# Performance work log

Hardware: AMD Instinct MI355X
Metric: run time of the kernel (lower is better)

The kernel has to match this reference:

```python
import jax, jax.numpy as jnp
import numpy as np

EPS = 1e-6          # VN leaky-relu denominator eps (vn_layers.py)
NEG_SLOPE = 0.2     # VNLinearLeakyReLU default negative_slope
K = 3               # pointops.interpolation default k
DIST_EPS = 1e-8     # interpolation inverse-distance eps


def vn_linear_leakyrelu(x, w_feat, w_dir):
    # x: [B, Cin, 3, N]; w_*: [Cout, Cin]  (bias-free Linears over channel dim)
    p = jnp.einsum('oc,bcvn->bovn', w_feat, x)
    d = jnp.einsum('oc,bcvn->bovn', w_dir, x)
    dot = jnp.sum(p * d, axis=2, keepdims=True)          # [B,Cout,1,N]
    d2 = jnp.sum(d * d, axis=2, keepdims=True)
    mask = (dot >= 0).astype(x.dtype)
    proj = p - (dot / (d2 + EPS)) * d                    # reflect negative part onto plane perp to d
    return NEG_SLOPE * p + (1.0 - NEG_SLOPE) * (mask * p + (1.0 - mask) * proj)


def interpolation(p2, p1, feat, b, n2, n1):
    # p2: [b*n2,3] coarse coords, p1: [b*n1,3] fine coords, feat: [C,3,b*n2]
    # k-NN inverse-squared-distance interpolation, segment-local per cloud.
    C = feat.shape[0]
    p2b = p2.reshape(b, n2, 3)
    p1b = p1.reshape(b, n1, 3)
    featb = feat.reshape(C * 3, b, n2).transpose(1, 2, 0)  # [b, n2, C*3]

    def per_batch(q, s, f):
        d2 = jnp.sum((q[:, None, :] - s[None, :, :]) ** 2, axis=-1)  # [n1,n2]
        neg_d2, idx = jax.lax.top_k(-d2, K)                          # k smallest sq-dists
        w = 1.0 / (-neg_d2 + DIST_EPS)
        w = w / jnp.sum(w, axis=1, keepdims=True)                    # [n1,K]
        return jnp.einsum('nk,nkc->nc', w, f[idx])                   # [n1, C*3]

    out = jax.vmap(per_batch)(p1b, p2b, featb)                       # [b, n1, C*3]
    return out.reshape(b, n1, C, 3).transpose(2, 3, 0, 1).reshape(C, 3, b * n1)


def setup_inputs() -> dict:
    key = jax.random.key(0)
    ks = jax.random.split(key, 8)
    b, n1, n2 = 4, 16384, 4096
    in_planes, out_planes = 128, 64
    p1 = jax.random.uniform(ks[0], (b * n1, 3), dtype=jnp.float32)
    p2 = jax.random.uniform(ks[1], (b * n2, 3), dtype=jnp.float32)
    x1 = jax.random.normal(ks[2], (1, out_planes, 3, b * n1), dtype=jnp.float32)
    x2 = jax.random.normal(ks[3], (1, in_planes, 3, b * n2), dtype=jnp.float32)
    o1 = (jnp.arange(1, b + 1, dtype=jnp.int32)) * n1   # cumulative offsets
    o2 = (jnp.arange(1, b + 1, dtype=jnp.int32)) * n2
    s1 = 1.0 / np.sqrt(out_planes)
    s2 = 1.0 / np.sqrt(in_planes)
    w1_feat = jax.random.uniform(ks[4], (out_planes, out_planes), jnp.float32, -s1, s1)
    w1_dir = jax.random.uniform(ks[5], (out_planes, out_planes), jnp.float32, -s1, s1)
    w2_feat = jax.random.uniform(ks[6], (out_planes, in_planes), jnp.float32, -s2, s2)
    w2_dir = jax.random.uniform(ks[7], (out_planes, in_planes), jnp.float32, -s2, s2)
    return {"p1": p1, "x1": x1, "o1": o1, "p2": p2, "x2": x2, "o2": o2,
            "w1_feat": w1_feat, "w1_dir": w1_dir, "w2_feat": w2_feat, "w2_dir": w2_dir}


def reference(p1, x1, o1, p2, x2, o2, w1_feat, w1_dir, w2_feat, w2_dir):
    b = o1.shape[0]
    n1 = x1.shape[-1] // b
    n2 = x2.shape[-1] // b
    y1 = vn_linear_leakyrelu(x1, w1_feat, w1_dir)            # [1,Cout,3,N1]
    y2 = vn_linear_leakyrelu(x2, w2_feat, w2_dir)[0]         # squeeze(0) -> [Cout,3,N2]
    up = interpolation(p2, p1, y2, b, n2, n1)                # [Cout,3,N1]
    return y1 + up
```

## Files before the change

kernel.cpp:

```cpp
#include <hip/hip_runtime.h>

#define N1T 65536
#define N2T 16384
#define COUT 64
#define CH 192
#define GRD 8
#define HCELL 0.125f

typedef unsigned short bhalf;
typedef __attribute__((ext_vector_type(8))) short short8;
typedef __attribute__((ext_vector_type(4))) float f32x4;

__device__ __forceinline__ bhalf f2bf(float f) {
    unsigned u = __float_as_uint(f);
    return (bhalf)((u + 0x7FFFu + ((u >> 16) & 1u)) >> 16);
}
__device__ __forceinline__ float bf2f(bhalf h) {
    return __uint_as_float(((unsigned)h) << 16);
}

__global__ __launch_bounds__(256) void wconv_kernel(
    const float* __restrict__ w1f, const float* __restrict__ w1d,
    const float* __restrict__ w2f, const float* __restrict__ w2d,
    bhalf* __restrict__ o1fh, bhalf* __restrict__ o1fl,
    bhalf* __restrict__ o1dh, bhalf* __restrict__ o1dl,
    bhalf* __restrict__ o2fh, bhalf* __restrict__ o2fl,
    bhalf* __restrict__ o2dh, bhalf* __restrict__ o2dl) {
    const int i = blockIdx.x * 256 + threadIdx.x;
    if (i < 4096) {
        const float a = w1f[i]; const bhalf ah = f2bf(a);
        o1fh[i] = ah; o1fl[i] = f2bf(a - bf2f(ah));
        const float b = w1d[i]; const bhalf bh = f2bf(b);
        o1dh[i] = bh; o1dl[i] = f2bf(b - bf2f(bh));
    }
    const float a = w2f[i]; const bhalf ah = f2bf(a);
    o2fh[i] = ah; o2fl[i] = f2bf(a - bf2f(ah));
    const float b = w2d[i]; const bhalf bh = f2bf(b);
    o2dh[i] = bh; o2dl[i] = f2bf(b - bf2f(bh));
}

template<int CIN, int N, bool CM>
__global__ __launch_bounds__(512) void vn_mfma_kernel(
    const float* __restrict__ x,
    const bhalf* __restrict__ wfh, const bhalf* __restrict__ wfl,
    const bhalf* __restrict__ wdh, const bhalf* __restrict__ wdl,
    const int*   __restrict__ idxs,
    const float* __restrict__ wts,
    const float* __restrict__ y2t,
    float* __restrict__ out)
{
    constexpr int ROWS = CIN * 3;
    constexpr int LDSC = CIN * 3 + 8;
    __shared__ __align__(16) bhalf xs_h[32][LDSC];
    __shared__ __align__(16) bhalf xs_l[32][LDSC];

    const int tid  = threadIdx.x;
    const int lane = tid & 63;
    const int wave = tid >> 6;
    const int n0   = blockIdx.x * 32;
    const int r16  = lane & 15;
    const int hh   = lane >> 4;
    const int ot   = wave & 3;
    const int sW   = wave >> 2;
    const int pt   = sW * 16 + r16;
    const int n    = n0 + pt;

    int gk[3]; float gw[3];
    if constexpr (CM) {
#pragma unroll
        for (int r = 0; r < 3; ++r) {
            gk[r] = idxs[r * N1T + n];
            gw[r] = wts[r * N1T + n];
        }
    }

    constexpr int NF4 = ROWS * 8;
    for (int i4 = tid; i4 < NF4; i4 += 512) {
        const int row = i4 >> 3, p4 = i4 & 7;
        const float4 v = *(const float4*)&x[(size_t)row * N + n0 + p4 * 4];
        const int c = row / 3, vv = row - c * 3;
        const int colS = (vv * CIN + c) ^ ((p4 & 3) << 3);
        const float vals[4] = {v.x, v.y, v.z, v.w};
#pragma unroll
        for (int j = 0; j < 4; ++j) {
            const bhalf h = f2bf(vals[j]);
            xs_h[p4*4+j][colS] = h;
            xs_l[p4*4+j][colS] = f2bf(vals[j] - bf2f(h));
        }
    }
    __syncthreads();

    const f32x4 zero = {0.f, 0.f, 0.f, 0.f};
    f32x4 accP[3], accD[3];
#pragma unroll
    for (int v = 0; v < 3; ++v) { accP[v] = zero; accD[v] = zero; }

    const int wofs = (ot * 16 + r16) * CIN + hh * 8;
    const bhalf* __restrict__ pfh = wfh + wofs;
    const bhalf* __restrict__ pfl = wfl + wofs;
    const bhalf* __restrict__ pdh = wdh + wofs;
    const bhalf* __restrict__ pdl = wdl + wofs;

    const int hs = ((hh ^ (r16 >> 2)) & 3) * 8 + (hh & ~3) * 8;
#pragma unroll
    for (int k = 0; k < CIN / 32; ++k) {
        const short8 afh = *(const short8*)(pfh + k * 32);
        const short8 afl = *(const short8*)(pfl + k * 32);
        const short8 adh = *(const short8*)(pdh + k * 32);
        const short8 adl = *(const short8*)(pdl + k * 32);
#pragma unroll
        for (int v = 0; v < 3; ++v) {
            const short8 bh = *(const short8*)&xs_h[pt][v * CIN + k * 32 + hs];
            const short8 bl = *(const short8*)&xs_l[pt][v * CIN + k * 32 + hs];
            accP[v] = __builtin_amdgcn_mfma_f32_16x16x32_bf16(afh, bh, accP[v], 0, 0, 0);
            accP[v] = __builtin_amdgcn_mfma_f32_16x16x32_bf16(afl, bh, accP[v], 0, 0, 0);
            accP[v] = __builtin_amdgcn_mfma_f32_16x16x32_bf16(afh, bl, accP[v], 0, 0, 0);
            accD[v] = __builtin_amdgcn_mfma_f32_16x16x32_bf16(adh, bh, accD[v], 0, 0, 0);
            accD[v] = __builtin_amdgcn_mfma_f32_16x16x32_bf16(adl, bh, accD[v], 0, 0, 0);
            accD[v] = __builtin_amdgcn_mfma_f32_16x16x32_bf16(adh, bl, accD[v], 0, 0, 0);
        }
    }

    float rr[12];
#pragma unroll
    for (int reg = 0; reg < 4; ++reg) {
        const float p0 = accP[0][reg], p1 = accP[1][reg], p2 = accP[2][reg];
        const float q0 = accD[0][reg], q1 = accD[1][reg], q2 = accD[2][reg];
        const float dot = p0*q0 + p1*q1 + p2*q2;
        const float dd  = q0*q0 + q1*q1 + q2*q2;
        const float coef = (dot < 0.f) ? (0.8f * dot / (dd + 1e-6f)) : 0.f;
        rr[reg*3+0] = p0 - coef * q0;
        rr[reg*3+1] = p1 - coef * q1;
        rr[reg*3+2] = p2 - coef * q2;
    }

    if constexpr (!CM) {
        float* op = out + (size_t)n * CH + ot * 48 + hh * 12;
        *(float4*)&op[0] = make_float4(rr[0], rr[1], rr[2],  rr[3]);
        *(float4*)&op[4] = make_float4(rr[4], rr[5], rr[6],  rr[7]);
        *(float4*)&op[8] = make_float4(rr[8], rr[9], rr[10], rr[11]);
    } else {
        const int chb = ot * 48 + hh * 12;
        const float* __restrict__ r0 = y2t + (size_t)gk[0] * CH + chb;
        const float* __restrict__ r1 = y2t + (size_t)gk[1] * CH + chb;
        const float* __restrict__ r2 = y2t + (size_t)gk[2] * CH + chb;
        const float w0 = gw[0], w1 = gw[1], w2 = gw[2];
        float4 a0[3], a1[3], a2[3];
#pragma unroll
        for (int q = 0; q < 3; ++q) {
            a0[q] = *(const float4*)&r0[q * 4];
            a1[q] = *(const float4*)&r1[q * 4];
            a2[q] = *(const float4*)&r2[q * 4];
        }
#pragma unroll
        for (int q = 0; q < 3; ++q) {
            const float u0 = w0*a0[q].x + w1*a1[q].x + w2*a2[q].x;
            const float u1 = w0*a0[q].y + w1*a1[q].y + w2*a2[q].y;
            const float u2 = w0*a0[q].z + w1*a1[q].z + w2*a2[q].z;
            const float u3 = w0*a0[q].w + w1*a1[q].w + w2*a2[q].w;
            out[(size_t)(chb + q*4 + 0) * N + n] = rr[q*4+0] + u0;
            out[(size_t)(chb + q*4 + 1) * N + n] = rr[q*4+1] + u1;
            out[(size_t)(chb + q*4 + 2) * N + n] = rr[q*4+2] + u2;
            out[(size_t)(chb + q*4 + 3) * N + n] = rr[q*4+3] + u3;
        }
    }
}

#define KNN_INSERT(d2, j)                                        \
    {                                                            \
        const bool c0 = (d2) < b0;                               \
        const bool c1 = (d2) < b1;                               \
        const bool c2 = (d2) < b2v;                              \
        const float nb2 = c2 ? (c1 ? b1 : (d2)) : b2v;           \
        const int   ni2 = c2 ? (c1 ? i1 : (j))  : i2;            \
        const float nb1 = c1 ? (c0 ? b0 : (d2)) : b1;            \
        const int   ni1 = c1 ? (c0 ? i0 : (j))  : i1;            \
        b0 = c0 ? (d2) : b0;  i0 = c0 ? (j) : i0;                \
        b1 = nb1; i1 = ni1; b2v = nb2; i2 = ni2;                 \
    }

__global__ __launch_bounds__(256) void zero_kernel(int* __restrict__ p, int n) {
    const int i = blockIdx.x * 256 + threadIdx.x;
    if (i < n) p[i] = 0;
}

__device__ __forceinline__ int cell_of(float x, float y, float z) {
    int cx = (int)(x * (float)GRD); cx = cx < 0 ? 0 : (cx > GRD-1 ? GRD-1 : cx);
    int cy = (int)(y * (float)GRD); cy = cy < 0 ? 0 : (cy > GRD-1 ? GRD-1 : cy);
    int cz = (int)(z * (float)GRD); cz = cz < 0 ? 0 : (cz > GRD-1 ? GRD-1 : cz);
    return (cz << 6) | (cy << 3) | cx;
}

__global__ __launch_bounds__(256) void bin_count_kernel(
    const float* __restrict__ p2, int* __restrict__ counts) {
    const int i = blockIdx.x * 256 + threadIdx.x;
    const float x = p2[i*3+0], y = p2[i*3+1], z = p2[i*3+2];
    const int cell = ((i >> 12) << 9) | cell_of(x, y, z);
    atomicAdd(&counts[cell], 1);
}

__global__ __launch_bounds__(256) void scan_kernel(
    const int* __restrict__ counts, int* __restrict__ off) {
    __shared__ int buf[2][256];
    const int t = threadIdx.x;
    int v[8]; int s = 0;
#pragma unroll
    for (int j = 0; j < 8; ++j) { const int tmp = counts[t*8+j]; v[j] = s; s += tmp; }
    buf[0][t] = s; __syncthreads();
    int src = 0;
    for (int d = 1; d < 256; d <<= 1) {
        int val = buf[src][t];
        if (t >= d) val += buf[src][t - d];
        buf[src ^ 1][t] = val; src ^= 1; __syncthreads();
    }
    const int incl = buf[src][t];
    const int base = incl - s;
#pragma unroll
    for (int j = 0; j < 8; ++j) off[t*8+j] = base + v[j];
    if (t == 255) off[2048] = incl;
}

__global__ __launch_bounds__(256) void bin_scatter_kernel(
    const float* __restrict__ p2, const int* __restrict__ off,
    int* __restrict__ cnt2, float4* __restrict__ binned) {
    const int i = blockIdx.x * 256 + threadIdx.x;
    const float x = p2[i*3+0], y = p2[i*3+1], z = p2[i*3+2];
    const int cell = ((i >> 12) << 9) | cell_of(x, y, z);
    const int pos = off[cell] + atomicAdd(&cnt2[cell], 1);
    binned[pos] = make_float4(x, y, z, __int_as_float(i));
}

__global__ __launch_bounds__(256) void knn_grid_kernel(
    const float* __restrict__ p1,
    const float4* __restrict__ binned,
    const int* __restrict__ off,
    int*   __restrict__ idx_out,
    float* __restrict__ w_out)
{
    const int t   = blockIdx.x * 256 + threadIdx.x;
    const int fp  = t >> 2;
    const int sub = t & 3;
    const int bi  = fp >> 14;
    const int cbase = bi << 9;

    const float qx = p1[fp*3+0], qy = p1[fp*3+1], qz = p1[fp*3+2];
    int cx = (int)(qx * (float)GRD); cx = cx < 0 ? 0 : (cx > 7 ? 7 : cx);
    int cy = (int)(qy * (float)GRD); cy = cy < 0 ? 0 : (cy > 7 ? 7 : cy);
    int cz = (int)(qz * (float)GRD); cz = cz < 0 ? 0 : (cz > 7 ? 7 : cz);

    float b0 = 1e30f, b1 = 1e30f, b2v = 1e30f;
    int   i0 = 0,     i1 = 0,     i2 = 0;

    for (int dz = -1; dz <= 1; ++dz)
    for (int dy = -1; dy <= 1; ++dy)
    for (int dx = -1; dx <= 1; ++dx) {
        const int nx = cx + dx, ny = cy + dy, nz = cz + dz;
        if ((unsigned)nx > 7u || (unsigned)ny > 7u || (unsigned)nz > 7u) continue;
        const int c = cbase + (nz << 6) + (ny << 3) + nx;
        const int s = off[c], e = off[c + 1];
        for (int k = s + sub; k < e; k += 4) {
            const float4 c4 = binned[k];
            const float ddx = qx - c4.x, ddy = qy - c4.y, ddz = qz - c4.z;
            const float d2 = fmaf(ddx, ddx, fmaf(ddy, ddy, ddz * ddz));
            const int j = __float_as_int(c4.w);
            KNN_INSERT(d2, j)
        }
    }

#pragma unroll
    for (int m = 1; m <= 2; m <<= 1) {
        const float c0v = __shfl_xor(b0, m, 4);
        const float c1v = __shfl_xor(b1, m, 4);
        const float c2v = __shfl_xor(b2v, m, 4);
        const int   j0v = __shfl_xor(i0, m, 4);
        const int   j1v = __shfl_xor(i1, m, 4);
        const int   j2v = __shfl_xor(i2, m, 4);
        KNN_INSERT(c0v, j0v)
        KNN_INSERT(c1v, j1v)
        KNN_INSERT(c2v, j2v)
    }

    float dw = 1e30f;
    if (cx >= 2) dw = fminf(dw, qx - (float)(cx - 1) * HCELL);
    if (cx <= 5) dw = fminf(dw, (float)(cx + 2) * HCELL - qx);
    if (cy >= 2) dw = fminf(dw, qy - (float)(cy - 1) * HCELL);
    if (cy <= 5) dw = fminf(dw, (float)(cy + 2) * HCELL - qy);
    if (cz >= 2) dw = fminf(dw, qz - (float)(cz - 1) * HCELL);
    if (cz <= 5) dw = fminf(dw, (float)(cz + 2) * HCELL - qz);
    const bool done = b2v < dw * dw;

    if (!done) {
        b0 = b1 = b2v = 1e30f; i0 = i1 = i2 = 0;
        const int s = bi << 12, e = (bi + 1) << 12;
        for (int k = s + sub; k < e; k += 4) {
            const float4 c4 = binned[k];
            const float ddx = qx - c4.x, ddy = qy - c4.y, ddz = qz - c4.z;
            const float d2 = fmaf(ddx, ddx, fmaf(ddy, ddy, ddz * ddz));
            const int j = __float_as_int(c4.w);
            KNN_INSERT(d2, j)
        }
#pragma unroll
        for (int m = 1; m <= 2; m <<= 1) {
            const float c0v = __shfl_xor(b0, m, 4);
            const float c1v = __shfl_xor(b1, m, 4);
            const float c2v = __shfl_xor(b2v, m, 4);
            const int   j0v = __shfl_xor(i0, m, 4);
            const int   j1v = __shfl_xor(i1, m, 4);
            const int   j2v = __shfl_xor(i2, m, 4);
            KNN_INSERT(c0v, j0v)
            KNN_INSERT(c1v, j1v)
            KNN_INSERT(c2v, j2v)
        }
    }

    if (sub == 0) {
        const float w0 = 1.f / (b0 + 1e-8f);
        const float w1 = 1.f / (b1 + 1e-8f);
        const float w2 = 1.f / (b2v + 1e-8f);
        const float inv = 1.f / (w0 + w1 + w2);
        idx_out[0*N1T + fp] = i0;
        idx_out[1*N1T + fp] = i1;
        idx_out[2*N1T + fp] = i2;
        w_out[0*N1T + fp] = w0 * inv;
        w_out[1*N1T + fp] = w1 * inv;
        w_out[2*N1T + fp] = w2 * inv;
    }
}

extern "C" void kernel_launch(void* const* d_in, const int* in_sizes, int n_in,
                              void* d_out, int out_size, void* d_ws, size_t ws_size,
                              hipStream_t stream) {
    const float* p1      = (const float*)d_in[0];
    const float* x1      = (const float*)d_in[1];
    const float* p2      = (const float*)d_in[3];
    const float* x2      = (const float*)d_in[4];
    const float* w1_feat = (const float*)d_in[6];
    const float* w1_dir  = (const float*)d_in[7];
    const float* w2_feat = (const float*)d_in[8];
    const float* w2_dir  = (const float*)d_in[9];
    float* out = (float*)d_out;

    char* ws = (char*)d_ws;
    float*  y2t    = (float*)ws;                 ws += (size_t)N2T * CH * 4;
    int*    idxs   = (int*)ws;                   ws += (size_t)3 * N1T * 4;
    float*  wts    = (float*)ws;                 ws += (size_t)3 * N1T * 4;
    int*    counts = (int*)ws;                   ws += 2048 * 4;
    int*    cnt2   = (int*)ws;                   ws += 2048 * 4;
    int*    off    = (int*)ws;                   ws += 2064 * 4;
    float4* binned = (float4*)ws;                ws += (size_t)N2T * 16;
    bhalf*  wb1fh  = (bhalf*)ws;                 ws += 4096 * 2;
    bhalf*  wb1fl  = (bhalf*)ws;                 ws += 4096 * 2;
    bhalf*  wb1dh  = (bhalf*)ws;                 ws += 4096 * 2;
    bhalf*  wb1dl  = (bhalf*)ws;                 ws += 4096 * 2;
    bhalf*  wb2fh  = (bhalf*)ws;                 ws += 8192 * 2;
    bhalf*  wb2fl  = (bhalf*)ws;                 ws += 8192 * 2;
    bhalf*  wb2dh  = (bhalf*)ws;                 ws += 8192 * 2;
    bhalf*  wb2dl  = (bhalf*)ws;                 ws += 8192 * 2;

    wconv_kernel<<<32, 256, 0, stream>>>(w1_feat, w1_dir, w2_feat, w2_dir,
                                         wb1fh, wb1fl, wb1dh, wb1dl,
                                         wb2fh, wb2fl, wb2dh, wb2dl);

    zero_kernel<<<16, 256, 0, stream>>>(counts, 4096);
    bin_count_kernel<<<N2T/256, 256, 0, stream>>>(p2, counts);
    scan_kernel<<<1, 256, 0, stream>>>(counts, off);
    bin_scatter_kernel<<<N2T/256, 256, 0, stream>>>(p2, off, cnt2, binned);
    knn_grid_kernel<<<(4*N1T)/256, 256, 0, stream>>>(p1, binned, off, idxs, wts);

    vn_mfma_kernel<128, N2T, false><<<N2T/32, 512, 0, stream>>>(
        x2, wb2fh, wb2fl, wb2dh, wb2dl, nullptr, nullptr, nullptr, y2t);
    vn_mfma_kernel<64, N1T, true><<<N1T/32, 512, 0, stream>>>(
        x1, wb1fh, wb1fl, wb1dh, wb1dl, idxs, wts, y2t, out);
}
```

Baseline: 105.6 us.

## Process two point tiles per block with double-buffered LDS prefetch

The final VN MFMA kernel now handles two 32-point tiles per block. It loads the second tile's input into registers while the first tile is computed, then writes it into a second LDS buffer. This aims to hide global load latency behind MFMA work and to reuse weights across tiles. In exchange, the grid is halved, LDS per block doubles, and register pressure rises, which may reduce occupancy.

Result: no change. 104.5 us (-1.0%).

```diff
diff --git a/kernel.cpp b/kernel.cpp
--- a/kernel.cpp
+++ b/kernel.cpp
@@ -39,7 +39,7 @@
     o2dh[i] = bh; o2dl[i] = f2bf(b - bf2f(bh));
 }
 
-template<int CIN, int N, bool CM>
+template<int CIN, int N, bool CM, int NT>
 __global__ __launch_bounds__(512) void vn_mfma_kernel(
     const float* __restrict__ x,
     const bhalf* __restrict__ wfh, const bhalf* __restrict__ wfl,
@@ -51,118 +51,146 @@
 {
     constexpr int ROWS = CIN * 3;
     constexpr int LDSC = CIN * 3 + 8;
-    __shared__ __align__(16) bhalf xs_h[32][LDSC];
-    __shared__ __align__(16) bhalf xs_l[32][LDSC];
+    constexpr int NB   = (NT > 1) ? 2 : 1;
+    constexpr int NLD  = ROWS * 8 / 512;
+    __shared__ __align__(16) bhalf xs_h[NB][32][LDSC];
+    __shared__ __align__(16) bhalf xs_l[NB][32][LDSC];
 
     const int tid  = threadIdx.x;
     const int lane = tid & 63;
     const int wave = tid >> 6;
-    const int n0   = blockIdx.x * 32;
     const int r16  = lane & 15;
     const int hh   = lane >> 4;
     const int ot   = wave & 3;
     const int sW   = wave >> 2;
     const int pt   = sW * 16 + r16;
-    const int n    = n0 + pt;
-
-    int gk[3]; float gw[3];
+    const int tile0 = blockIdx.x * NT;
+
+    int gk[NT][3]; float gw[NT][3];
     if constexpr (CM) {
 #pragma unroll
-        for (int r = 0; r < 3; ++r) {
-            gk[r] = idxs[r * N1T + n];
-            gw[r] = wts[r * N1T + n];
-        }
-    }
-
-    constexpr int NF4 = ROWS * 8;
-    for (int i4 = tid; i4 < NF4; i4 += 512) {
-        const int row = i4 >> 3, p4 = i4 & 7;
-        const float4 v = *(const float4*)&x[(size_t)row * N + n0 + p4 * 4];
-        const int c = row / 3, vv = row - c * 3;
-        const int colS = (vv * CIN + c) ^ ((p4 & 3) << 3);
-        const float vals[4] = {v.x, v.y, v.z, v.w};
-#pragma unroll
-        for (int j = 0; j < 4; ++j) {
-            const bhalf h = f2bf(vals[j]);
-            xs_h[p4*4+j][colS] = h;
-            xs_l[p4*4+j][colS] = f2bf(vals[j] - bf2f(h));
-        }
-    }
-    __syncthreads();
-
-    const f32x4 zero = {0.f, 0.f, 0.f, 0.f};
-    f32x4 accP[3], accD[3];
-#pragma unroll
-    for (int v = 0; v < 3; ++v) { accP[v] = zero; accD[v] = zero; }
+        for (int t = 0; t < NT; ++t) {
+            const int n = (tile0 + t) * 32 + pt;
+#pragma unroll
+            for (int r = 0; r < 3; ++r) {
+                gk[t][r] = idxs[r * N1T + n];
+                gw[t][r] = wts[r * N1T + n];
+            }
+        }
+    }
 
     const int wofs = (ot * 16 + r16) * CIN + hh * 8;
     const bhalf* __restrict__ pfh = wfh + wofs;
     const bhalf* __restrict__ pfl = wfl + wofs;
     const bhalf* __restrict__ pdh = wdh + wofs;
     const bhalf* __restrict__ pdl = wdl + wofs;
-
-    const int hs = ((hh ^ (r16 >> 2)) & 3) * 8 + (hh & ~3) * 8;
-#pragma unroll
-    for (int k = 0; k < CIN / 32; ++k) {
-        const short8 afh = *(const short8*)(pfh + k * 32);
-        const short8 afl = *(const short8*)(pfl + k * 32);
-        const short8 adh = *(const short8*)(pdh + k * 32);
-        const short8 adl = *(const short8*)(pdl + k * 32);
-#pragma unroll
-        for (int v = 0; v < 3; ++v) {
-            const short8 bh = *(const short8*)&xs_h[pt][v * CIN + k * 32 + hs];
-            const short8 bl = *(const short8*)&xs_l[pt][v * CIN + k * 32 + hs];
-            accP[v] = __builtin_amdgcn_mfma_f32_16x16x32_bf16(afh, bh, accP[v], 0, 0, 0);
-            accP[v] = __builtin_amdgcn_mfma_f32_16x16x32_bf16(afl, bh, accP[v], 0, 0, 0);
-            accP[v] = __builtin_amdgcn_mfma_f32_16x16x32_bf16(afh, bl, accP[v], 0, 0, 0);
-            accD[v] = __builtin_amdgcn_mfma_f32_16x16x32_bf16(adh, bh, accD[v], 0, 0, 0);
-            accD[v] = __builtin_amdgcn_mfma_f32_16x16x32_bf16(adl, bh, accD[v], 0, 0, 0);
-            accD[v] = __builtin_amdgcn_mfma_f32_16x16x32_bf16(adh, bl, accD[v], 0, 0, 0);
-        }
-    }
-
-    float rr[12];
-#pragma unroll
-    for (int reg = 0; reg < 4; ++reg) {
-        const float p0 = accP[0][reg], p1 = accP[1][reg], p2 = accP[2][reg];
-        const float q0 = accD[0][reg], q1 = accD[1][reg], q2 = accD[2][reg];
-        const float dot = p0*q0 + p1*q1 + p2*q2;
-        const float dd  = q0*q0 + q1*q1 + q2*q2;
-        const float coef = (dot < 0.f) ? (0.8f * dot / (dd + 1e-6f)) : 0.f;
-        rr[reg*3+0] = p0 - coef * q0;
-        rr[reg*3+1] = p1 - coef * q1;
-        rr[reg*3+2] = p2 - coef * q2;
-    }
-
-    if constexpr (!CM) {
-        float* op = out + (size_t)n * CH + ot * 48 + hh * 12;
-        *(float4*)&op[0] = make_float4(rr[0], rr[1], rr[2],  rr[3]);
-        *(float4*)&op[4] = make_float4(rr[4], rr[5], rr[6],  rr[7]);
-        *(float4*)&op[8] = make_float4(rr[8], rr[9], rr[10], rr[11]);
+    const int hs = ((hh ^ (r16 >> 2)) & 3) * 8;
+
+    auto LOADT = [&](float4 (&st)[NLD], int t) {
+#pragma unroll
+        for (int r = 0; r < NLD; ++r) {
+            const int i4 = r * 512 + tid;
+            const int row = i4 >> 3, p4 = i4 & 7;
+            st[r] = *(const float4*)&x[(size_t)row * N + (size_t)(tile0 + t) * 32 + p4 * 4];
+        }
+    };
+    auto WRITET = [&](const float4 (&st)[NLD], int b) {
+#pragma unroll
+        for (int r = 0; r < NLD; ++r) {
+            const int i4 = r * 512 + tid;
+            const int row = i4 >> 3, p4 = i4 & 7;
+            const int c = row / 3, vv = row - c * 3;
+            const int colS = (vv * CIN + c) ^ ((p4 & 3) << 3);
+            const float vals[4] = {st[r].x, st[r].y, st[r].z, st[r].w};
+#pragma unroll
+            for (int j = 0; j < 4; ++j) {
+                const bhalf h = f2bf(vals[j]);
+                xs_h[b][p4*4+j][colS] = h;
+                xs_l[b][p4*4+j][colS] = f2bf(vals[j] - bf2f(h));
+            }
+        }
+    };
+    auto COMPUTET = [&](int t, int b, const int (&gkt)[3], const float (&gwt)[3]) {
+        const f32x4 zero = {0.f, 0.f, 0.f, 0.f};
+        f32x4 accP[3], accD[3];
+#pragma unroll
+        for (int v = 0; v < 3; ++v) { accP[v] = zero; accD[v] = zero; }
+#pragma unroll
+        for (int k = 0; k < CIN / 32; ++k) {
+            const short8 afh = *(const short8*)(pfh + k * 32);
+            const short8 afl = *(const short8*)(pfl + k * 32);
+            const short8 adh = *(const short8*)(pdh + k * 32);
+            const short8 adl = *(const short8*)(pdl + k * 32);
+#pragma unroll
+            for (int v = 0; v < 3; ++v) {
+                const short8 bh = *(const short8*)&xs_h[b][pt][v * CIN + k * 32 + hs];
+                const short8 bl = *(const short8*)&xs_l[b][pt][v * CIN + k * 32 + hs];
+                accP[v] = __builtin_amdgcn_mfma_f32_16x16x32_bf16(afh, bh, accP[v], 0, 0, 0);
+                accP[v] = __builtin_amdgcn_mfma_f32_16x16x32_bf16(afl, bh, accP[v], 0, 0, 0);
+                accP[v] = __builtin_amdgcn_mfma_f32_16x16x32_bf16(afh, bl, accP[v], 0, 0, 0);
+                accD[v] = __builtin_amdgcn_mfma_f32_16x16x32_bf16(adh, bh, accD[v], 0, 0, 0);
+                accD[v] = __builtin_amdgcn_mfma_f32_16x16x32_bf16(adl, bh, accD[v], 0, 0, 0);
+                accD[v] = __builtin_amdgcn_mfma_f32_16x16x32_bf16(adh, bl, accD[v], 0, 0, 0);
+            }
+        }
+        float rr[12];
+#pragma unroll
+        for (int reg = 0; reg < 4; ++reg) {
+            const float p0 = accP[0][reg], p1 = accP[1][reg], p2 = accP[2][reg];
+            const float q0 = accD[0][reg], q1 = accD[1][reg], q2 = accD[2][reg];
+            const float dot = p0*q0 + p1*q1 + p2*q2;
+            const float dd  = q0*q0 + q1*q1 + q2*q2;
+            const float coef = (dot < 0.f) ? (0.8f * dot / (dd + 1e-6f)) : 0.f;
+            rr[reg*3+0] = p0 - coef * q0;
+            rr[reg*3+1] = p1 - coef * q1;
+            rr[reg*3+2] = p2 - coef * q2;
+        }
+        const int n = (tile0 + t) * 32 + pt;
+        if constexpr (!CM) {
+            float* op = out + (size_t)n * CH + ot * 48 + hh * 12;
+            *(float4*)&op[0] = make_float4(rr[0], rr[1], rr[2],  rr[3]);
+            *(float4*)&op[4] = make_float4(rr[4], rr[5], rr[6],  rr[7]);
+            *(float4*)&op[8] = make_float4(rr[8], rr[9], rr[10], rr[11]);
+        } else {
+            const int chb = ot * 48 + hh * 12;
+            const float* __restrict__ r0 = y2t + (size_t)gkt[0] * CH + chb;
+            const float* __restrict__ r1 = y2t + (size_t)gkt[1] * CH + chb;
+            const float* __restrict__ r2 = y2t + (size_t)gkt[2] * CH + chb;
+            const float w0 = gwt[0], w1 = gwt[1], w2 = gwt[2];
+            float4 a0[3], a1[3], a2[3];
+#pragma unroll
+            for (int q = 0; q < 3; ++q) {
+                a0[q] = *(const float4*)&r0[q * 4];
+                a1[q] = *(const float4*)&r1[q * 4];
+                a2[q] = *(const float4*)&r2[q * 4];
+            }
+#pragma unroll
+            for (int q = 0; q < 3; ++q) {
+                const float u0 = w0*a0[q].x + w1*a1[q].x + w2*a2[q].x;
+                const float u1 = w0*a0[q].y + w1*a1[q].y + w2*a2[q].y;
+                const float u2 = w0*a0[q].z + w1*a1[q].z + w2*a2[q].z;
+                const float u3 = w0*a0[q].w + w1*a1[q].w + w2*a2[q].w;
+                out[(size_t)(chb + q*4 + 0) * N + n] = rr[q*4+0] + u0;
+                out[(size_t)(chb + q*4 + 1) * N + n] = rr[q*4+1] + u1;
+                out[(size_t)(chb + q*4 + 2) * N + n] = rr[q*4+2] + u2;
+                out[(size_t)(chb + q*4 + 3) * N + n] = rr[q*4+3] + u3;
+            }
+        }
+    };
+
+    float4 stA[NLD], stB[NLD];
+    LOADT(stA, 0);
+    WRITET(stA, 0);
+    if constexpr (NT == 2) {
+        LOADT(stB, 1);
+        __syncthreads();
+        COMPUTET(0, 0, gk[0], gw[0]);
+        WRITET(stB, 1);
+        __syncthreads();
+        COMPUTET(1, 1, gk[1], gw[1]);
     } else {
-        const int chb = ot * 48 + hh * 12;
-        const float* __restrict__ r0 = y2t + (size_t)gk[0] * CH + chb;
-        const float* __restrict__ r1 = y2t + (size_t)gk[1] * CH + chb;
-        const float* __restrict__ r2 = y2t + (size_t)gk[2] * CH + chb;
-        const float w0 = gw[0], w1 = gw[1], w2 = gw[2];
-        float4 a0[3], a1[3], a2[3];
-#pragma unroll
-        for (int q = 0; q < 3; ++q) {
-            a0[q] = *(const float4*)&r0[q * 4];
-            a1[q] = *(const float4*)&r1[q * 4];
-            a2[q] = *(const float4*)&r2[q * 4];
-        }
-#pragma unroll
-        for (int q = 0; q < 3; ++q) {
-            const float u0 = w0*a0[q].x + w1*a1[q].x + w2*a2[q].x;
-            const float u1 = w0*a0[q].y + w1*a1[q].y + w2*a2[q].y;
-            const float u2 = w0*a0[q].z + w1*a1[q].z + w2*a2[q].z;
-            const float u3 = w0*a0[q].w + w1*a1[q].w + w2*a2[q].w;
-            out[(size_t)(chb + q*4 + 0) * N + n] = rr[q*4+0] + u0;
-            out[(size_t)(chb + q*4 + 1) * N + n] = rr[q*4+1] + u1;
-            out[(size_t)(chb + q*4 + 2) * N + n] = rr[q*4+2] + u2;
-            out[(size_t)(chb + q*4 + 3) * N + n] = rr[q*4+3] + u3;
-        }
+        __syncthreads();
+        COMPUTET(0, 0, gk[0], gw[0]);
     }
 }
 
@@ -367,8 +395,8 @@
     bin_scatter_kernel<<<N2T/256, 256, 0, stream>>>(p2, off, cnt2, binned);
     knn_grid_kernel<<<(4*N1T)/256, 256, 0, stream>>>(p1, binned, off, idxs, wts);
 
-    vn_mfma_kernel<128, N2T, false><<<N2T/32, 512, 0, stream>>>(
+    vn_mfma_kernel<128, N2T, false, 1><<<N2T/32, 512, 0, stream>>>(
         x2, wb2fh, wb2fl, wb2dh, wb2dl, nullptr, nullptr, nullptr, y2t);
-    vn_mfma_kernel<64, N1T, true><<<N1T/32, 512, 0, stream>>>(
+    vn_mfma_kernel<64, N1T, true, 2><<<N1T/64, 512, 0, stream>>>(
         x1, wb1fh, wb1fl, wb1dh, wb1dl, idxs, wts, y2t, out);
 }
```

## Load VN1 inputs directly into registers, merge kNN x-row cell scans

Applied to the files above, without the earlier changes.

The first-layer VN kernel no longer stages its inputs in LDS. Each wave loads its point's channel values straight from global memory into registers, splits them into bf16 hi/lo parts by truncation, and issues the gathers for the interpolation rows early so they overlap with the MFMA work. This removes the LDS round trip and the block-wide barrier, at the cost of strided per-lane global loads and more register pressure. The kNN search now scans each row of three neighbouring x-cells as one contiguous range, using 9 offset lookups instead of 27, and the second-layer kernel's load loop gets a fixed unrolled trip count.

Result: slower. 112.4 us (+6.4%).

```diff
diff --git a/kernel.cpp b/kernel.cpp
--- a/kernel.cpp
+++ b/kernel.cpp
@@ -39,8 +39,27 @@
     o2dh[i] = bh; o2dl[i] = f2bf(b - bf2f(bh));
 }
 
-template<int CIN, int N, bool CM>
-__global__ __launch_bounds__(512) void vn_mfma_kernel(
+__device__ __forceinline__ void pack_split(const float (&f)[8], short8& bh, short8& bl) {
+    union { short8 s; uint4 u; } ch, cl;
+    unsigned hd[4], ld[4];
+#pragma unroll
+    for (int m = 0; m < 4; ++m) {
+        const unsigned u0 = __float_as_uint(f[2*m]);
+        const unsigned u1 = __float_as_uint(f[2*m+1]);
+        const unsigned h0 = u0 & 0xFFFF0000u;
+        const unsigned h1 = u1 & 0xFFFF0000u;
+        hd[m] = (h0 >> 16) | h1;
+        const float l0 = f[2*m]   - __uint_as_float(h0);
+        const float l1 = f[2*m+1] - __uint_as_float(h1);
+        ld[m] = (__float_as_uint(l0) >> 16) | (__float_as_uint(l1) & 0xFFFF0000u);
+    }
+    ch.u = make_uint4(hd[0], hd[1], hd[2], hd[3]);
+    cl.u = make_uint4(ld[0], ld[1], ld[2], ld[3]);
+    bh = ch.s; bl = cl.s;
+}
+
+template<int N>
+__global__ __launch_bounds__(256) void vn1_fused_kernel(
     const float* __restrict__ x,
     const bhalf* __restrict__ wfh, const bhalf* __restrict__ wfl,
     const bhalf* __restrict__ wdh, const bhalf* __restrict__ wdl,
@@ -49,33 +68,128 @@
     const float* __restrict__ y2t,
     float* __restrict__ out)
 {
+    constexpr int CIN = 64;
+    const int lane  = threadIdx.x & 63;
+    const int gid   = (blockIdx.x * 256 + threadIdx.x) >> 6;
+    const int ptile = gid >> 2;
+    const int ot    = gid & 3;
+    const int r16   = lane & 15;
+    const int hh    = lane >> 4;
+    const int n     = ptile * 16 + r16;
+    const int chb   = ot * 48 + hh * 12;
+
+    const int   gk0 = idxs[0*N1T + n], gk1 = idxs[1*N1T + n], gk2 = idxs[2*N1T + n];
+    const float w0  = wts[0*N1T + n],  w1  = wts[1*N1T + n],  w2  = wts[2*N1T + n];
+
+    const float* __restrict__ xb = x + (size_t)(hh * 24) * N + n;
+    float xf[2][3][8];
+#pragma unroll
+    for (int k = 0; k < 2; ++k)
+#pragma unroll
+        for (int v = 0; v < 3; ++v)
+#pragma unroll
+            for (int j = 0; j < 8; ++j)
+                xf[k][v][j] = xb[(size_t)(k * 96 + j * 3 + v) * N];
+
+    const int wofs = (ot * 16 + r16) * CIN + hh * 8;
+    short8 afh[2], afl[2], adh[2], adl[2];
+#pragma unroll
+    for (int k = 0; k < 2; ++k) {
+        afh[k] = *(const short8*)(wfh + wofs + k * 32);
+        afl[k] = *(const short8*)(wfl + wofs + k * 32);
+        adh[k] = *(const short8*)(wdh + wofs + k * 32);
+        adl[k] = *(const short8*)(wdl + wofs + k * 32);
+    }
+
+    const float* __restrict__ r0p = y2t + (size_t)gk0 * CH + chb;
+    const float* __restrict__ r1p = y2t + (size_t)gk1 * CH + chb;
+    const float* __restrict__ r2p = y2t + (size_t)gk2 * CH + chb;
+    float4 g0[3], g1[3], g2[3];
+#pragma unroll
+    for (int q = 0; q < 3; ++q) {
+        g0[q] = *(const float4*)&r0p[q * 4];
+        g1[q] = *(const float4*)&r1p[q * 4];
+        g2[q] = *(const float4*)&r2p[q * 4];
+    }
+
+    const f32x4 zero = {0.f, 0.f, 0.f, 0.f};
+    f32x4 accP[3], accD[3];
+#pragma unroll
+    for (int v = 0; v < 3; ++v) { accP[v] = zero; accD[v] = zero; }
+#pragma unroll
+    for (int k = 0; k < 2; ++k) {
+#pragma unroll
+        for (int v = 0; v < 3; ++v) {
+            short8 bh, bl;
+            pack_split(xf[k][v], bh, bl);
+            accP[v] = __builtin_amdgcn_mfma_f32_16x16x32_bf16(afh[k], bh, accP[v], 0, 0, 0);
+            accP[v] = __builtin_amdgcn_mfma_f32_16x16x32_bf16(afl[k], bh, accP[v], 0, 0, 0);
+            accP[v] = __builtin_amdgcn_mfma_f32_16x16x32_bf16(afh[k], bl, accP[v], 0, 0, 0);
+            accD[v] = __builtin_amdgcn_mfma_f32_16x16x32_bf16(adh[k], bh, accD[v], 0, 0, 0);
+            accD[v] = __builtin_amdgcn_mfma_f32_16x16x32_bf16(adl[k], bh, accD[v], 0, 0, 0);
+            accD[v] = __builtin_amdgcn_mfma_f32_16x16x32_bf16(adh[k], bl, accD[v], 0, 0, 0);
+        }
+    }
+
+    float rr[12];
+#pragma unroll
+    for (int reg = 0; reg < 4; ++reg) {
+        const float p0 = accP[0][reg], p1 = accP[1][reg], p2 = accP[2][reg];
+        const float q0 = accD[0][reg], q1 = accD[1][reg], q2 = accD[2][reg];
+        const float dot = p0*q0 + p1*q1 + p2*q2;
+        const float dd  = q0*q0 + q1*q1 + q2*q2;
+        const float coef = (dot < 0.f) ? (0.8f * dot / (dd + 1e-6f)) : 0.f;
+        rr[reg*3+0] = p0 - coef * q0;
+        rr[reg*3+1] = p1 - coef * q1;
+        rr[reg*3+2] = p2 - coef * q2;
+    }
+
+#pragma unroll
+    for (int q = 0; q < 3; ++q) {
+        const float u0 = w0*g0[q].x + w1*g1[q].x + w2*g2[q].x;
+        const float u1 = w0*g0[q].y + w1*g1[q].y + w2*g2[q].y;
+        const float u2 = w0*g0[q].z + w1*g1[q].z + w2*g2[q].z;
+        const float u3 = w0*g0[q].w + w1*g1[q].w + w2*g2[q].w;
+        out[(size_t)(chb + q*4 + 0) * N + n] = rr[q*4+0] + u0;
+        out[(size_t)(chb + q*4 + 1) * N + n] = rr[q*4+1] + u1;
+        out[(size_t)(chb + q*4 + 2) * N + n] = rr[q*4+2] + u2;
+        out[(size_t)(chb + q*4 + 3) * N + n] = rr[q*4+3] + u3;
+    }
+}
+
+template<int CIN, int N>
+__global__ __launch_bounds__(512) void vn_mfma_kernel(
+    const float* __restrict__ x,
+    const bhalf* __restrict__ wfh, const bhalf* __restrict__ wfl,
+    const bhalf* __restrict__ wdh, const bhalf* __restrict__ wdl,
+    float* __restrict__ out)
+{
     constexpr int ROWS = CIN * 3;
     constexpr int LDSC = CIN * 3 + 8;
+    constexpr int NLD  = ROWS * 8 / 512;
     __shared__ __align__(16) bhalf xs_h[32][LDSC];
     __shared__ __align__(16) bhalf xs_l[32][LDSC];
 
     const int tid  = threadIdx.x;
     const int lane = tid & 63;
     const int wave = tid >> 6;
-    const int n0   = blockIdx.x * 32;
     const int r16  = lane & 15;
     const int hh   = lane >> 4;
     const int ot   = wave & 3;
     const int sW   = wave >> 2;
     const int pt   = sW * 16 + r16;
-    const int n    = n0 + pt;
-
-    int gk[3]; float gw[3];
-    if constexpr (CM) {
-#pragma unroll
-        for (int r = 0; r < 3; ++r) {
-            gk[r] = idxs[r * N1T + n];
-            gw[r] = wts[r * N1T + n];
-        }
-    }
-
-    constexpr int NF4 = ROWS * 8;
-    for (int i4 = tid; i4 < NF4; i4 += 512) {
+    const int n0   = blockIdx.x * 32;
+
+    const int wofs = (ot * 16 + r16) * CIN + hh * 8;
+    const bhalf* __restrict__ pfh = wfh + wofs;
+    const bhalf* __restrict__ pfl = wfl + wofs;
+    const bhalf* __restrict__ pdh = wdh + wofs;
+    const bhalf* __restrict__ pdl = wdl + wofs;
+    const int hs = ((hh ^ (r16 >> 2)) & 3) * 8;
+
+#pragma unroll
+    for (int r = 0; r < NLD; ++r) {
+        const int i4 = r * 512 + tid;
         const int row = i4 >> 3, p4 = i4 & 7;
         const float4 v = *(const float4*)&x[(size_t)row * N + n0 + p4 * 4];
         const int c = row / 3, vv = row - c * 3;
@@ -94,14 +208,6 @@
     f32x4 accP[3], accD[3];
 #pragma unroll
     for (int v = 0; v < 3; ++v) { accP[v] = zero; accD[v] = zero; }
-
-    const int wofs = (ot * 16 + r16) * CIN + hh * 8;
-    const bhalf* __restrict__ pfh = wfh + wofs;
-    const bhalf* __restrict__ pfl = wfl + wofs;
-    const bhalf* __restrict__ pdh = wdh + wofs;
-    const bhalf* __restrict__ pdl = wdl + wofs;
-
-    const int hs = ((hh ^ (r16 >> 2)) & 3) * 8 + (hh & ~3) * 8;
 #pragma unroll
     for (int k = 0; k < CIN / 32; ++k) {
         const short8 afh = *(const short8*)(pfh + k * 32);
@@ -133,37 +239,11 @@
         rr[reg*3+1] = p1 - coef * q1;
         rr[reg*3+2] = p2 - coef * q2;
     }
-
-    if constexpr (!CM) {
-        float* op = out + (size_t)n * CH + ot * 48 + hh * 12;
-        *(float4*)&op[0] = make_float4(rr[0], rr[1], rr[2],  rr[3]);
-        *(float4*)&op[4] = make_float4(rr[4], rr[5], rr[6],  rr[7]);
-        *(float4*)&op[8] = make_float4(rr[8], rr[9], rr[10], rr[11]);
-    } else {
-        const int chb = ot * 48 + hh * 12;
-        const float* __restrict__ r0 = y2t + (size_t)gk[0] * CH + chb;
-        const float* __restrict__ r1 = y2t + (size_t)gk[1] * CH + chb;
-        const float* __restrict__ r2 = y2t + (size_t)gk[2] * CH + chb;
-        const float w0 = gw[0], w1 = gw[1], w2 = gw[2];
-        float4 a0[3], a1[3], a2[3];
-#pragma unroll
-        for (int q = 0; q < 3; ++q) {
-            a0[q] = *(const float4*)&r0[q * 4];
-            a1[q] = *(const float4*)&r1[q * 4];
-            a2[q] = *(const float4*)&r2[q * 4];
-        }
-#pragma unroll
-        for (int q = 0; q < 3; ++q) {
-            const float u0 = w0*a0[q].x + w1*a1[q].x + w2*a2[q].x;
-            const float u1 = w0*a0[q].y + w1*a1[q].y + w2*a2[q].y;
-            const float u2 = w0*a0[q].z + w1*a1[q].z + w2*a2[q].z;
-            const float u3 = w0*a0[q].w + w1*a1[q].w + w2*a2[q].w;
-            out[(size_t)(chb + q*4 + 0) * N + n] = rr[q*4+0] + u0;
-            out[(size_t)(chb + q*4 + 1) * N + n] = rr[q*4+1] + u1;
-            out[(size_t)(chb + q*4 + 2) * N + n] = rr[q*4+2] + u2;
-            out[(size_t)(chb + q*4 + 3) * N + n] = rr[q*4+3] + u3;
-        }
-    }
+    const int n = n0 + pt;
+    float* op = out + (size_t)n * CH + ot * 48 + hh * 12;
+    *(float4*)&op[0] = make_float4(rr[0], rr[1], rr[2],  rr[3]);
+    *(float4*)&op[4] = make_float4(rr[4], rr[5], rr[6],  rr[7]);
+    *(float4*)&op[8] = make_float4(rr[8], rr[9], rr[10], rr[11]);
 }
 
 #define KNN_INSERT(d2, j)                                        \
@@ -248,22 +328,29 @@
     int cy = (int)(qy * (float)GRD); cy = cy < 0 ? 0 : (cy > 7 ? 7 : cy);
     int cz = (int)(qz * (float)GRD); cz = cz < 0 ? 0 : (cz > 7 ? 7 : cz);
 
+    const int x0 = cx > 0 ? cx - 1 : 0;
+    const int x1 = cx < 7 ? cx + 1 : 7;
+
     float b0 = 1e30f, b1 = 1e30f, b2v = 1e30f;
     int   i0 = 0,     i1 = 0,     i2 = 0;
 
-    for (int dz = -1; dz <= 1; ++dz)
-    for (int dy = -1; dy <= 1; ++dy)
-    for (int dx = -1; dx <= 1; ++dx) {
-        const int nx = cx + dx, ny = cy + dy, nz = cz + dz;
-        if ((unsigned)nx > 7u || (unsigned)ny > 7u || (unsigned)nz > 7u) continue;
-        const int c = cbase + (nz << 6) + (ny << 3) + nx;
-        const int s = off[c], e = off[c + 1];
-        for (int k = s + sub; k < e; k += 4) {
-            const float4 c4 = binned[k];
-            const float ddx = qx - c4.x, ddy = qy - c4.y, ddz = qz - c4.z;
-            const float d2 = fmaf(ddx, ddx, fmaf(ddy, ddy, ddz * ddz));
-            const int j = __float_as_int(c4.w);
-            KNN_INSERT(d2, j)
+#pragma unroll
+    for (int dz = -1; dz <= 1; ++dz) {
+        const int nz = cz + dz;
+        if ((unsigned)nz > 7u) continue;
+#pragma unroll
+        for (int dy = -1; dy <= 1; ++dy) {
+            const int ny = cy + dy;
+            if ((unsigned)ny > 7u) continue;
+            const int cb = cbase + (nz << 6) + (ny << 3);
+            const int s = off[cb + x0], e = off[cb + x1 + 1];
+            for (int k = s + sub; k < e; k += 4) {
+                const float4 c4 = binned[k];
+                const float ddx = qx - c4.x, ddy = qy - c4.y, ddz = qz - c4.z;
+                const float d2 = fmaf(ddx, ddx, fmaf(ddy, ddy, ddz * ddz));
+                const int j = __float_as_int(c4.w);
+                KNN_INSERT(d2, j)
+            }
         }
     }
 
@@ -367,8 +454,8 @@
     bin_scatter_kernel<<<N2T/256, 256, 0, stream>>>(p2, off, cnt2, binned);
     knn_grid_kernel<<<(4*N1T)/256, 256, 0, stream>>>(p1, binned, off, idxs, wts);
 
-    vn_mfma_kernel<128, N2T, false><<<N2T/32, 512, 0, stream>>>(
-        x2, wb2fh, wb2fl, wb2dh, wb2dl, nullptr, nullptr, nullptr, y2t);
-    vn_mfma_kernel<64, N1T, true><<<N1T/32, 512, 0, stream>>>(
+    vn_mfma_kernel<128, N2T><<<N2T/32, 512, 0, stream>>>(
+        x2, wb2fh, wb2fl, wb2dh, wb2dl, y2t);
+    vn1_fused_kernel<N1T><<<(N1T/16)*4/4, 256, 0, stream>>>(
         x1, wb1fh, wb1fl, wb1dh, wb1dl, idxs, wts, y2t, out);
 }
```
